# Optimization experiments

Measured on AMD Instinct MI355X. Metric: run time of the kernel, lower is better.

The kernel has to match this reference:

```python
import jax, jax.numpy as jnp
import numpy as np

FRACTAL_OUTPUT = (5, 5)            # (a, b); requires 5 * num_kernels == a*b
PERC_THRESHOLD = 0.59275
NEXT_SHAPE = (224, 224)
K_END = int(0.4 * FRACTAL_OUTPUT[0] * FRACTAL_OUTPUT[1] + 1)   # 11
KERNEL_SIZES = list(range(3, K_END + 1, 2))                    # [3,5,7,9,11]


def setup_inputs() -> dict:
    key = jax.random.key(0)
    inputs = jax.random.uniform(key, (64, 224, 224, 3), dtype=jnp.float32) * 255.0
    return {"inputs": inputs}


def _extract_patches(x, k):
    # tf.image.extract_patches(sizes=strides=k, SAME) == zero-pad + space-to-depth
    B, H, W, C = x.shape
    rows, cols = -(-H // k), -(-W // k)
    ph, pw = rows * k - H, cols * k - W
    x = jnp.pad(x, ((0, 0), (ph // 2, ph - ph // 2), (pw // 2, pw - pw // 2), (0, 0)))
    x = x.reshape(B, rows, k, cols, k, C).transpose(0, 1, 3, 2, 4, 5)
    return x.reshape(B * rows * cols, k, k, C), rows * cols


def _binarize(patches, k, ch):
    # distance function: 1 iff |channel value - center pixel channel value| <= k
    center = patches[:, k // 2, k // 2, ch][:, None, None]
    return (jnp.abs(patches[..., ch] - center) <= k).astype(jnp.int32)


def _connected_stats(binp, k):
    # 4-connected components via min-label propagation (== tfa connected_components
    # up to relabeling; we only need #components and max label count incl. background)
    N = binp.shape[0]
    idx = jnp.arange(1, k * k + 1, dtype=jnp.int32).reshape(k, k)
    INF = jnp.int32(k * k + 2)
    lbl0 = jnp.where(binp > 0, idx, 0)

    def step(_, lbl):
        v = jnp.where(binp > 0, lbl, INF)
        pad = lambda a, w: jnp.pad(a, ((0, 0),) + w, constant_values=INF)
        up    = pad(v, ((1, 0), (0, 0)))[:, :-1, :]
        down  = pad(v, ((0, 1), (0, 0)))[:, 1:, :]
        left  = pad(v, ((0, 0), (1, 0)))[:, :, :-1]
        right = pad(v, ((0, 0), (0, 1)))[:, :, 1:]
        m = jnp.minimum(jnp.minimum(v, up), jnp.minimum(jnp.minimum(down, left), right))
        return jnp.where(binp > 0, m, 0)

    lbl = jax.lax.fori_loop(0, k * k, step, lbl0)  # k*k iters guarantee convergence
    ncomp = jnp.sum((binp > 0) & (lbl == idx), axis=(1, 2)).astype(jnp.int32)
    lblf = lbl.reshape(N, k * k)
    cnt = jnp.zeros((N, k * k + 1), jnp.int32).at[jnp.arange(N)[:, None], lblf].add(1)
    return ncomp, cnt.max(axis=1)  # (#components, most-common label count incl bg 0)


def _components(inputs, k, ch):
    B = inputs.shape[0]
    patches, P = _extract_patches(inputs, k)
    binp = _binarize(patches, k, ch)                    # (B*P, k, k)
    ones = binp.sum(axis=(1, 2)).reshape(B, P)          # int counts per patch
    # tf.bincount(minlength=1, maxlength=k*k): bins 0..k*k-1, value k*k dropped
    cnt = jnp.zeros((B, k * k + 1), jnp.float32).at[jnp.arange(B)[:, None], ones].add(1.0)
    prob = cnt[:, : k * k] / P                          # (B, k*k)
    n = jnp.arange(1, k * k + 1, dtype=jnp.float32)
    fd = (prob / n).sum(1)
    m = (prob * n).sum(1)
    m2 = ((prob * prob) * n).sum(1)
    lac = (m2 - m * m) / (m * m)
    perc = ((ones.astype(jnp.float32) / (k * k)) >= PERC_THRESHOLD).astype(jnp.int32)
    acp = perc.sum(1) // P                              # tf integer reduce_mean
    ncomp, marea = _connected_stats(binp, k)
    acn = ncomp.reshape(B, P).sum(1) // P
    acma = marea.reshape(B, P).sum(1) // P
    return jnp.stack([acn.astype(jnp.float32), acp.astype(jnp.float32),
                      acma.astype(jnp.float32), lac, fd], axis=1)   # (B, 5)


def _rearrange(c):
    # group metric-major: all acn over kernels, then acp, acma, lac, fd
    return jnp.concatenate([c[:, mm::5] for mm in range(5)], axis=1)


def reference(inputs):
    B = inputs.shape[0]
    chans = []
    for ch in range(3):
        comps = jnp.concatenate([_components(inputs, k, ch) for k in KERNEL_SIZES], axis=1)
        chans.append(_rearrange(comps).reshape(B, FRACTAL_OUTPUT[0], FRACTAL_OUTPUT[1]))
    out = jnp.stack(chans, axis=3)                      # (B, a, b, 3)
    return jax.image.resize(out, (B, NEXT_SHAPE[0], NEXT_SHAPE[1], 3), method='bilinear')
```

## Files before the change

### kernel.cpp

```cpp
#include <hip/hip_runtime.h>

#define HW 224
#define NIMG 64
#define NPIX ((size_t)NIMG * HW * HW)

struct U128 { unsigned long long lo, hi; };
__device__ __forceinline__ U128 u_or  (U128 a, U128 b){ return {a.lo|b.lo, a.hi|b.hi}; }
__device__ __forceinline__ U128 u_and (U128 a, U128 b){ return {a.lo&b.lo, a.hi&b.hi}; }
__device__ __forceinline__ U128 u_andn(U128 a, U128 b){ return {a.lo&~b.lo, a.hi&~b.hi}; }
__device__ __forceinline__ bool u_eq(U128 a, U128 b){ return a.lo==b.lo && a.hi==b.hi; }
__device__ __forceinline__ bool u_nz(U128 a){ return (a.lo | a.hi) != 0ull; }
__device__ __forceinline__ U128 u_shl(U128 a, int n){
    return { a.lo << n, (a.hi << n) | (a.lo >> (64 - n)) };
}
__device__ __forceinline__ U128 u_shr(U128 a, int n){
    return { (a.lo >> n) | (a.hi << (64 - n)), a.hi >> n };
}
__device__ __forceinline__ int u_pop(U128 a){ return __popcll(a.lo) + __popcll(a.hi); }
__device__ __forceinline__ U128 u_low(U128 a){
    if (a.lo) return { a.lo & (0ull - a.lo), 0ull };
    return { 0ull, a.hi & (0ull - a.hi) };
}


template<int K, int S>
__device__ __forceinline__ void stats_body(const float* __restrict__ img,
                                           float* __restrict__ o,
                                           int hist[4][124], int* sums) {
    constexpr int KK   = K * K;
    constexpr int ROWS = (HW + K - 1) / K;
    constexpr int P    = ROWS * ROWS;
    constexpr int PAD  = (ROWS * K - HW) / 2;
    const int wid = threadIdx.x >> 6;

    U128 leftCol{0,0}, rightCol{0,0};
#pragma unroll
    for (int i = 0; i < K; i++) {
        const int cl = i * K, cr = i * K + K - 1;
        if (cl < 64) leftCol.lo  |= 1ull << cl; else leftCol.hi  |= 1ull << (cl - 64);
        if (cr < 64) rightCol.lo |= 1ull << cr; else rightCol.hi |= 1ull << (cr - 64);
    }

    int t_perc = 0, t_ncomp = 0, t_marea = 0;

    for (int p = threadIdx.x; p < P; p += 256) {
        const int pr = p / ROWS, pc = p - pr * ROWS;
        const int y0 = pr * K - PAD, x0 = pc * K - PAD;
        const float cen = img[((size_t)(y0 + K / 2) * HW + (x0 + K / 2)) * S];

        U128 msk{0, 0};
#pragma unroll
        for (int i = 0; i < K; i++) {
            const int y = y0 + i;
            const bool yin = (unsigned)y < (unsigned)HW;
#pragma unroll
            for (int j = 0; j < K; j++) {
                const int x = x0 + j;
                const bool inb = yin && ((unsigned)x < (unsigned)HW);
                const float v = inb ? img[((size_t)y * HW + x) * S] : 0.0f;
                const unsigned long long bit = (fabsf(v - cen) <= (float)K) ? 1ull : 0ull;
                const int c = i * K + j;
                if (c < 64) msk.lo |= bit << c; else msk.hi |= bit << (c - 64);
            }
        }
        const int ones = u_pop(msk);

        int ncomp = 0, maxsz = 0;
        U128 m = msk;
        while (u_nz(m)) {
            U128 s = u_low(m);
            for (;;) {
                U128 g = s;
                g = u_or(g, u_shl(u_andn(s, rightCol), 1));
                g = u_or(g, u_shr(u_andn(s, leftCol), 1));
                g = u_or(g, u_shl(s, K));
                g = u_or(g, u_shr(s, K));
                g = u_and(g, m);
                if (u_eq(g, s)) break;
                s = g;
            }
            ncomp++;
            const int sz = u_pop(s);
            if (sz > maxsz) maxsz = sz;
            m = u_andn(m, s);
        }

        const int bgcnt = KK - ones;
        const int marea = (bgcnt > maxsz) ? bgcnt : maxsz;

        t_ncomp += ncomp;
        t_marea += marea;
        if ((float)ones / (float)KK >= 0.59275f) t_perc++;
        atomicAdd(&hist[wid][ones], 1);
    }

    atomicAdd(&sums[0], t_perc);
    atomicAdd(&sums[1], t_ncomp);
    atomicAdd(&sums[2], t_marea);
    __syncthreads();

    if (threadIdx.x == 0) {
        const float Pf = (float)P;
        float fd = 0.0f, m1 = 0.0f, m2 = 0.0f;
        for (int s = 0; s < KK; s++) {
            const float prob = (float)(hist[0][s] + hist[1][s] + hist[2][s] + hist[3][s]) / Pf;
            const float n = (float)(s + 1);
            fd += prob / n;
            m1 += prob * n;
            m2 += prob * prob * n;
        }
        const float lac = (m2 - m1 * m1) / (m1 * m1);
        o[0]  = (float)(sums[1] / P);
        o[15] = (float)(sums[0] / P);
        o[30] = (float)(sums[2] / P);
        o[45] = lac;
        o[60] = fd;
    }
}

template<int S>
__global__ __launch_bounds__(256) void fractal_stats(const float* __restrict__ in,
                                                     float* __restrict__ interm) {
    const int b    = blockIdx.x / 15;
    const int rem  = blockIdx.x % 15;
    const int ch   = rem / 5;
    const int kidx = rem % 5;

    __shared__ int hist[4][124];
    __shared__ int sums[3];
    for (int i = threadIdx.x; i < 4 * 124; i += 256) ((int*)hist)[i] = 0;
    if (threadIdx.x < 3) sums[threadIdx.x] = 0;
    __syncthreads();

    const float* img = (S == 1) ? in + ((size_t)ch * NIMG + b) * HW * HW
                                : in + (size_t)b * HW * HW * 3 + ch;
    float* o = interm + (size_t)b * 75 + kidx * 3 + ch;

    switch (kidx) {
        case 0: stats_body<3,  S>(img, o, hist, sums); break;
        case 1: stats_body<5,  S>(img, o, hist, sums); break;
        case 2: stats_body<7,  S>(img, o, hist, sums); break;
        case 3: stats_body<9,  S>(img, o, hist, sums); break;
        case 4: stats_body<11, S>(img, o, hist, sums); break;
    }
}

__global__ __launch_bounds__(256) void deinterleave(const float* __restrict__ in,
                                                    float* __restrict__ planes) {
    const size_t pix = (size_t)blockIdx.x * 256 + threadIdx.x;
    if (pix >= NPIX) return;
    const float v0 = in[pix * 3 + 0];
    const float v1 = in[pix * 3 + 1];
    const float v2 = in[pix * 3 + 2];
    planes[pix]            = v0;
    planes[NPIX + pix]     = v1;
    planes[2 * NPIX + pix] = v2;
}

__global__ __launch_bounds__(256) void fractal_resize(const float* __restrict__ interm,
                                                      float* __restrict__ out, int total) {
    const int idx = blockIdx.x * 256 + threadIdx.x;
    if (idx >= total) return;
    const int ch = idx % 3;
    int t = idx / 3;
    const int x = t % HW; t /= HW;
    const int y = t % HW;
    const int b = t / HW;

    const float sc = 5.0f / 224.0f;
    const float uy = ((float)y + 0.5f) * sc - 0.5f;
    const float ux = ((float)x + 0.5f) * sc - 0.5f;

    const float fy = floorf(uy), fx = floorf(ux);
    const float wy = uy - fy,    wx = ux - fx;
    int y0 = (int)fy, x0 = (int)fx;
    int y1 = y0 + 1,  x1 = x0 + 1;
    if (y0 < 0) y0 = 0; if (x0 < 0) x0 = 0;
    if (y1 > 4) y1 = 4; if (x1 > 4) x1 = 4;

    const float* g = interm + (size_t)b * 75 + ch;
    const float v00 = g[(y0 * 5 + x0) * 3];
    const float v01 = g[(y0 * 5 + x1) * 3];
    const float v10 = g[(y1 * 5 + x0) * 3];
    const float v11 = g[(y1 * 5 + x1) * 3];

    out[idx] = (1.0f - wy) * ((1.0f - wx) * v00 + wx * v01)
             +         wy  * ((1.0f - wx) * v10 + wx * v11);
}

extern "C" void kernel_launch(void* const* d_in, const int* in_sizes, int n_in,
                              void* d_out, int out_size, void* d_ws, size_t ws_size,
                              hipStream_t stream) {
    const float* in = (const float*)d_in[0];
    float* out = (float*)d_out;
    float* interm = (float*)d_ws;

    const size_t planes_off = 19456;
    const size_t need = planes_off + 3 * NPIX * sizeof(float);

    if (ws_size >= need) {
        float* planes = (float*)((char*)d_ws + planes_off);
        deinterleave<<<(int)((NPIX + 255) / 256), 256, 0, stream>>>(in, planes);
        fractal_stats<1><<<NIMG * 15, 256, 0, stream>>>(planes, interm);
    } else {
        fractal_stats<3><<<NIMG * 15, 256, 0, stream>>>(in, interm);
    }
    fractal_resize<<<(out_size + 255) / 256, 256, 0, stream>>>(interm, out, out_size);
}
```

Measured before the change: 185.8 us.

## Split each stats group across eight blocks with global atomic accumulation and finalize kernel

Each (image, channel, kernel-size) group is now spread over eight blocks, each taking a slice of the patches. Per-block histograms and sums are atomically added into a global accumulator, and a separate finalize kernel computes the metrics. Small kernels (K<=7) use a single 64-bit mask path instead of the 128-bit one. The deinterleave now handles four pixels per thread with float4 and also zeroes the accumulator. This fixes the poor occupancy of only 960 blocks with load imbalance, at the cost of an extra launch and global atomics.

```diff
diff --git a/kernel.cpp b/kernel.cpp
--- a/kernel.cpp
+++ b/kernel.cpp
@@ -3,6 +3,9 @@
 #define HW 224
 #define NIMG 64
 #define NPIX ((size_t)NIMG * HW * HW)
+#define NGROUP 960
+#define ACC_STRIDE 128
+#define NSUB 8
 
 struct U128 { unsigned long long lo, hi; };
 __device__ __forceinline__ U128 u_or  (U128 a, U128 b){ return {a.lo|b.lo, a.hi|b.hi}; }
@@ -25,64 +28,106 @@
 
 template<int K, int S>
 __device__ __forceinline__ void stats_body(const float* __restrict__ img,
-                                           float* __restrict__ o,
+                                           int* __restrict__ acc, int sub,
                                            int hist[4][124], int* sums) {
-    constexpr int KK   = K * K;
-    constexpr int ROWS = (HW + K - 1) / K;
-    constexpr int P    = ROWS * ROWS;
-    constexpr int PAD  = (ROWS * K - HW) / 2;
+    constexpr int KK    = K * K;
+    constexpr int ROWS  = (HW + K - 1) / K;
+    constexpr int P     = ROWS * ROWS;
+    constexpr int PAD   = (ROWS * K - HW) / 2;
+    constexpr int CHUNK = (P + NSUB - 1) / NSUB;
     const int wid = threadIdx.x >> 6;
-
-    U128 leftCol{0,0}, rightCol{0,0};
-#pragma unroll
-    for (int i = 0; i < K; i++) {
-        const int cl = i * K, cr = i * K + K - 1;
-        if (cl < 64) leftCol.lo  |= 1ull << cl; else leftCol.hi  |= 1ull << (cl - 64);
-        if (cr < 64) rightCol.lo |= 1ull << cr; else rightCol.hi |= 1ull << (cr - 64);
-    }
+    const int pstart = sub * CHUNK;
+    const int pend   = (pstart + CHUNK < P) ? pstart + CHUNK : P;
 
     int t_perc = 0, t_ncomp = 0, t_marea = 0;
 
-    for (int p = threadIdx.x; p < P; p += 256) {
+    for (int p = pstart + threadIdx.x; p < pend; p += 256) {
         const int pr = p / ROWS, pc = p - pr * ROWS;
         const int y0 = pr * K - PAD, x0 = pc * K - PAD;
-        const float cen = img[((size_t)(y0 + K / 2) * HW + (x0 + K / 2)) * S];
-
-        U128 msk{0, 0};
-#pragma unroll
-        for (int i = 0; i < K; i++) {
-            const int y = y0 + i;
-            const bool yin = (unsigned)y < (unsigned)HW;
-#pragma unroll
-            for (int j = 0; j < K; j++) {
-                const int x = x0 + j;
-                const bool inb = yin && ((unsigned)x < (unsigned)HW);
-                const float v = inb ? img[((size_t)y * HW + x) * S] : 0.0f;
-                const unsigned long long bit = (fabsf(v - cen) <= (float)K) ? 1ull : 0ull;
-                const int c = i * K + j;
-                if (c < 64) msk.lo |= bit << c; else msk.hi |= bit << (c - 64);
-            }
-        }
-        const int ones = u_pop(msk);
-
-        int ncomp = 0, maxsz = 0;
-        U128 m = msk;
-        while (u_nz(m)) {
-            U128 s = u_low(m);
-            for (;;) {
-                U128 g = s;
-                g = u_or(g, u_shl(u_andn(s, rightCol), 1));
-                g = u_or(g, u_shr(u_andn(s, leftCol), 1));
-                g = u_or(g, u_shl(s, K));
-                g = u_or(g, u_shr(s, K));
-                g = u_and(g, m);
-                if (u_eq(g, s)) break;
-                s = g;
-            }
-            ncomp++;
-            const int sz = u_pop(s);
-            if (sz > maxsz) maxsz = sz;
-            m = u_andn(m, s);
+        const float cen = img[((y0 + K / 2) * HW + (x0 + K / 2)) * S];
+
+        int ones, ncomp = 0, maxsz = 0;
+
+        if constexpr (KK <= 64) {
+            unsigned long long LCOL = 0ull, RCOL = 0ull;
+#pragma unroll
+            for (int i = 0; i < K; i++) { LCOL |= 1ull << (i * K); RCOL |= 1ull << (i * K + K - 1); }
+
+            unsigned long long msk = 0ull;
+#pragma unroll
+            for (int i = 0; i < K; i++) {
+                const int y = y0 + i;
+                const bool yin = (unsigned)y < (unsigned)HW;
+#pragma unroll
+                for (int j = 0; j < K; j++) {
+                    const int x = x0 + j;
+                    const bool inb = yin && ((unsigned)x < (unsigned)HW);
+                    const float v = inb ? img[(y * HW + x) * S] : 0.0f;
+                    const unsigned long long bit = (fabsf(v - cen) <= (float)K) ? 1ull : 0ull;
+                    msk |= bit << (i * K + j);
+                }
+            }
+            ones = __popcll(msk);
+
+            unsigned long long m = msk;
+            while (m) {
+                unsigned long long s = m & (0ull - m);
+                for (;;) {
+                    unsigned long long g = s | ((s & ~RCOL) << 1) | ((s & ~LCOL) >> 1)
+                                             | (s << K) | (s >> K);
+                    g &= m;
+                    if (g == s) break;
+                    s = g;
+                }
+                ncomp++;
+                const int sz = __popcll(s);
+                if (sz > maxsz) maxsz = sz;
+                m &= ~s;
+            }
+        } else {
+            U128 LCOL{0,0}, RCOL{0,0};
+#pragma unroll
+            for (int i = 0; i < K; i++) {
+                const int cl = i * K, cr = i * K + K - 1;
+                if (cl < 64) LCOL.lo |= 1ull << cl; else LCOL.hi |= 1ull << (cl - 64);
+                if (cr < 64) RCOL.lo |= 1ull << cr; else RCOL.hi |= 1ull << (cr - 64);
+            }
+
+            U128 msk{0, 0};
+#pragma unroll
+            for (int i = 0; i < K; i++) {
+                const int y = y0 + i;
+                const bool yin = (unsigned)y < (unsigned)HW;
+#pragma unroll
+                for (int j = 0; j < K; j++) {
+                    const int x = x0 + j;
+                    const bool inb = yin && ((unsigned)x < (unsigned)HW);
+                    const float v = inb ? img[(y * HW + x) * S] : 0.0f;
+                    const unsigned long long bit = (fabsf(v - cen) <= (float)K) ? 1ull : 0ull;
+                    const int c = i * K + j;
+                    if (c < 64) msk.lo |= bit << c; else msk.hi |= bit << (c - 64);
+                }
+            }
+            ones = u_pop(msk);
+
+            U128 m = msk;
+            while (u_nz(m)) {
+                U128 s = u_low(m);
+                for (;;) {
+                    U128 g = s;
+                    g = u_or(g, u_shl(u_andn(s, RCOL), 1));
+                    g = u_or(g, u_shr(u_andn(s, LCOL), 1));
+                    g = u_or(g, u_shl(s, K));
+                    g = u_or(g, u_shr(s, K));
+                    g = u_and(g, m);
+                    if (u_eq(g, s)) break;
+                    s = g;
+                }
+                ncomp++;
+                const int sz = u_pop(s);
+                if (sz > maxsz) maxsz = sz;
+                m = u_andn(m, s);
+            }
         }
 
         const int bgcnt = KK - ones;
@@ -99,32 +144,22 @@
     atomicAdd(&sums[2], t_marea);
     __syncthreads();
 
-    if (threadIdx.x == 0) {
-        const float Pf = (float)P;
-        float fd = 0.0f, m1 = 0.0f, m2 = 0.0f;
-        for (int s = 0; s < KK; s++) {
-            const float prob = (float)(hist[0][s] + hist[1][s] + hist[2][s] + hist[3][s]) / Pf;
-            const float n = (float)(s + 1);
-            fd += prob / n;
-            m1 += prob * n;
-            m2 += prob * prob * n;
-        }
-        const float lac = (m2 - m1 * m1) / (m1 * m1);
-        o[0]  = (float)(sums[1] / P);
-        o[15] = (float)(sums[0] / P);
-        o[30] = (float)(sums[2] / P);
-        o[45] = lac;
-        o[60] = fd;
-    }
+    for (int s = threadIdx.x; s < KK; s += 256) {
+        const int v = hist[0][s] + hist[1][s] + hist[2][s] + hist[3][s];
+        if (v) atomicAdd(&acc[s], v);
+    }
+    if (threadIdx.x < 3) atomicAdd(&acc[124 + threadIdx.x], sums[threadIdx.x]);
 }
 
 template<int S>
 __global__ __launch_bounds__(256) void fractal_stats(const float* __restrict__ in,
-                                                     float* __restrict__ interm) {
-    const int b    = blockIdx.x / 15;
-    const int rem  = blockIdx.x % 15;
-    const int ch   = rem / 5;
-    const int kidx = rem % 5;
+                                                     int* __restrict__ gacc) {
+    const int group = blockIdx.x >> 3;
+    const int sub   = blockIdx.x & 7;
+    const int b     = group / 15;
+    const int rem   = group % 15;
+    const int ch    = rem / 5;
+    const int kidx  = rem % 5;
 
     __shared__ int hist[4][124];
     __shared__ int sums[3];
@@ -134,27 +169,62 @@
 
     const float* img = (S == 1) ? in + ((size_t)ch * NIMG + b) * HW * HW
                                 : in + (size_t)b * HW * HW * 3 + ch;
+    int* acc = gacc + group * ACC_STRIDE;
+
+    switch (kidx) {
+        case 0: stats_body<3,  S>(img, acc, sub, hist, sums); break;
+        case 1: stats_body<5,  S>(img, acc, sub, hist, sums); break;
+        case 2: stats_body<7,  S>(img, acc, sub, hist, sums); break;
+        case 3: stats_body<9,  S>(img, acc, sub, hist, sums); break;
+        case 4: stats_body<11, S>(img, acc, sub, hist, sums); break;
+    }
+}
+
+__global__ __launch_bounds__(256) void fractal_finalize(const int* __restrict__ gacc,
+                                                        float* __restrict__ interm) {
+    const int g = blockIdx.x * 256 + threadIdx.x;
+    if (g >= NGROUP) return;
+    const int b = g / 15, rem = g % 15, ch = rem / 5, kidx = rem % 5;
+    const int k = 3 + 2 * kidx, kk = k * k;
+    const int rows = (HW + k - 1) / k;
+    const int P = rows * rows;
+    const int* acc = gacc + g * ACC_STRIDE;
+
+    float fd = 0.0f, m1 = 0.0f, m2 = 0.0f;
+    const float Pf = (float)P;
+    for (int s = 0; s < kk; s++) {
+        const float prob = (float)acc[s] / Pf;
+        const float n = (float)(s + 1);
+        fd += prob / n;
+        m1 += prob * n;
+        m2 += prob * prob * n;
+    }
+    const float lac = (m2 - m1 * m1) / (m1 * m1);
     float* o = interm + (size_t)b * 75 + kidx * 3 + ch;
-
-    switch (kidx) {
-        case 0: stats_body<3,  S>(img, o, hist, sums); break;
-        case 1: stats_body<5,  S>(img, o, hist, sums); break;
-        case 2: stats_body<7,  S>(img, o, hist, sums); break;
-        case 3: stats_body<9,  S>(img, o, hist, sums); break;
-        case 4: stats_body<11, S>(img, o, hist, sums); break;
-    }
-}
-
-__global__ __launch_bounds__(256) void deinterleave(const float* __restrict__ in,
-                                                    float* __restrict__ planes) {
-    const size_t pix = (size_t)blockIdx.x * 256 + threadIdx.x;
-    if (pix >= NPIX) return;
-    const float v0 = in[pix * 3 + 0];
-    const float v1 = in[pix * 3 + 1];
-    const float v2 = in[pix * 3 + 2];
-    planes[pix]            = v0;
-    planes[NPIX + pix]     = v1;
-    planes[2 * NPIX + pix] = v2;
+    o[0]  = (float)(acc[125] / P);
+    o[15] = (float)(acc[124] / P);
+    o[30] = (float)(acc[126] / P);
+    o[45] = lac;
+    o[60] = fd;
+}
+
+__global__ __launch_bounds__(256) void deinterleave4(const float* __restrict__ in,
+                                                     float* __restrict__ planes,
+                                                     int* __restrict__ gacc) {
+    const int tid = blockIdx.x * 256 + threadIdx.x;
+    if (tid < NGROUP * ACC_STRIDE) gacc[tid] = 0;
+    const size_t p0 = (size_t)tid * 4;
+    if (p0 >= NPIX) return;
+    const float4* src = (const float4*)(in + p0 * 3);
+    const float4 a = src[0], bq = src[1], c = src[2];
+    *(float4*)(planes + p0)            = make_float4(a.x, a.w, bq.z, c.y);
+    *(float4*)(planes + NPIX + p0)     = make_float4(a.y, bq.x, bq.w, c.z);
+    *(float4*)(planes + 2 * NPIX + p0) = make_float4(a.z, bq.y, c.x, c.w);
+}
+
+__global__ __launch_bounds__(256) void zero_accum(int* __restrict__ gacc) {
+    const int tid = blockIdx.x * 256 + threadIdx.x;
+    if (tid < NGROUP * ACC_STRIDE) gacc[tid] = 0;
 }
 
 __global__ __launch_bounds__(256) void fractal_resize(const float* __restrict__ interm,
@@ -194,16 +264,18 @@
     const float* in = (const float*)d_in[0];
     float* out = (float*)d_out;
     float* interm = (float*)d_ws;
-
-    const size_t planes_off = 19456;
-    const size_t need = planes_off + 3 * NPIX * sizeof(float);
+    int*   gacc   = (int*)((char*)d_ws + 19456);
+    float* planes = (float*)((char*)d_ws + 512000);
+
+    const size_t need = 512000 + 3 * NPIX * sizeof(float);
 
     if (ws_size >= need) {
-        float* planes = (float*)((char*)d_ws + planes_off);
-        deinterleave<<<(int)((NPIX + 255) / 256), 256, 0, stream>>>(in, planes);
-        fractal_stats<1><<<NIMG * 15, 256, 0, stream>>>(planes, interm);
+        deinterleave4<<<(int)(NPIX / 4 / 256), 256, 0, stream>>>(in, planes, gacc);
+        fractal_stats<1><<<NGROUP * NSUB, 256, 0, stream>>>(planes, gacc);
     } else {
-        fractal_stats<3><<<NIMG * 15, 256, 0, stream>>>(in, interm);
-    }
+        zero_accum<<<(NGROUP * ACC_STRIDE + 255) / 256, 256, 0, stream>>>(gacc);
+        fractal_stats<3><<<NGROUP * NSUB, 256, 0, stream>>>(in, gacc);
+    }
+    fractal_finalize<<<(NGROUP + 255) / 256, 256, 0, stream>>>(gacc, interm);
     fractal_resize<<<(out_size + 255) / 256, 256, 0, stream>>>(interm, out, out_size);
 }
```

Measured after the change: 264.8 us. 42.5% more time.

## Stage image row bands in LDS and drop deinterleave pre-pass

Applied to the files above, without the earlier changes.

Removes the separate deinterleave kernel and planar workspace copy. Each block now loads bands of NB*K image rows from the interleaved input with float4 loads, extracts its channel, and stores the band to LDS with zero padding. Patches then read from LDS instead of strided global memory. It also adds a 64-bit mask fast path for K<=7 and a wave-shuffle reduction for the final statistics. The cost is extra block syncs per band and each block redundantly reading all three channels' data.

```diff
diff --git a/kernel.cpp b/kernel.cpp
--- a/kernel.cpp
+++ b/kernel.cpp
@@ -2,7 +2,8 @@
 
 #define HW 224
 #define NIMG 64
-#define NPIX ((size_t)NIMG * HW * HW)
+#define NGROUP 960
+#define LDS_F4 1914
 
 struct U128 { unsigned long long lo, hi; };
 __device__ __forceinline__ U128 u_or  (U128 a, U128 b){ return {a.lo|b.lo, a.hi|b.hi}; }
@@ -23,75 +24,145 @@
 }
 
 
-template<int K, int S>
-__device__ __forceinline__ void stats_body(const float* __restrict__ img,
-                                           float* __restrict__ o,
-                                           int hist[4][124], int* sums) {
-    constexpr int KK   = K * K;
-    constexpr int ROWS = (HW + K - 1) / K;
-    constexpr int P    = ROWS * ROWS;
-    constexpr int PAD  = (ROWS * K - HW) / 2;
-    const int wid = threadIdx.x >> 6;
-
-    U128 leftCol{0,0}, rightCol{0,0};
-#pragma unroll
-    for (int i = 0; i < K; i++) {
-        const int cl = i * K, cr = i * K + K - 1;
-        if (cl < 64) leftCol.lo  |= 1ull << cl; else leftCol.hi  |= 1ull << (cl - 64);
-        if (cr < 64) rightCol.lo |= 1ull << cr; else rightCol.hi |= 1ull << (cr - 64);
-    }
+template<int K>
+__device__ __forceinline__ void stats_group(const float* __restrict__ imgbase,
+                                            int ch,
+                                            float* __restrict__ o,
+                                            float4* lds4, int (*hist)[124],
+                                            int* sums) {
+    constexpr int KK    = K * K;
+    constexpr int ROWS  = (HW + K - 1) / K;
+    constexpr int P     = ROWS * ROWS;
+    constexpr int PAD   = (ROWS * K - HW) / 2;
+    constexpr int NB    = (K==3) ? 6 : (K==5) ? 5 : (K==7) ? 4 : 3;
+    constexpr int NCYC  = (ROWS + NB - 1) / NB;
+    constexpr int R     = NB * K;
+    constexpr int LPAD4 = (PAD > 0) ? 1 : 0;
+    constexpr int LPAD  = 4 * LPAD4;
+    constexpr int OFF   = LPAD - PAD;
+    constexpr int ACT   = NB * ROWS;
+
+    float* ldsf = (float*)lds4;
+    const int tid = threadIdx.x;
+    const int wid = (tid >> 6) & 1;
+
+    for (int i = tid; i < 2 * 124; i += 256) ((int*)hist)[i] = 0;
+    if (tid < 3) sums[tid] = 0;
+    __syncthreads();
 
     int t_perc = 0, t_ncomp = 0, t_marea = 0;
 
-    for (int p = threadIdx.x; p < P; p += 256) {
-        const int pr = p / ROWS, pc = p - pr * ROWS;
-        const int y0 = pr * K - PAD, x0 = pc * K - PAD;
-        const float cen = img[((size_t)(y0 + K / 2) * HW + (x0 + K / 2)) * S];
-
-        U128 msk{0, 0};
-#pragma unroll
-        for (int i = 0; i < K; i++) {
-            const int y = y0 + i;
-            const bool yin = (unsigned)y < (unsigned)HW;
-#pragma unroll
-            for (int j = 0; j < K; j++) {
-                const int x = x0 + j;
-                const bool inb = yin && ((unsigned)x < (unsigned)HW);
-                const float v = inb ? img[((size_t)y * HW + x) * S] : 0.0f;
-                const unsigned long long bit = (fabsf(v - cen) <= (float)K) ? 1ull : 0ull;
-                const int c = i * K + j;
-                if (c < 64) msk.lo |= bit << c; else msk.hi |= bit << (c - 64);
+    for (int s = 0; s < NCYC; s++) {
+        const int gy0 = s * NB * K - PAD;
+
+        for (int i = tid; i < R * 56; i += 256) {
+            const int r = i / 56, t4 = i - r * 56;
+            const int gy = gy0 + r;
+            float4 v = {0.f, 0.f, 0.f, 0.f};
+            if ((unsigned)gy < (unsigned)HW) {
+                const float4* s4 = (const float4*)(imgbase + 3 * (gy * HW + 4 * t4));
+                const float4 A = s4[0], B = s4[1], C = s4[2];
+                v = (ch == 0) ? float4{A.x, A.w, B.z, C.y}
+                  : (ch == 1) ? float4{A.y, B.x, B.w, C.z}
+                              : float4{A.z, B.y, C.x, C.w};
             }
-        }
-        const int ones = u_pop(msk);
-
-        int ncomp = 0, maxsz = 0;
-        U128 m = msk;
-        while (u_nz(m)) {
-            U128 s = u_low(m);
-            for (;;) {
-                U128 g = s;
-                g = u_or(g, u_shl(u_andn(s, rightCol), 1));
-                g = u_or(g, u_shr(u_andn(s, leftCol), 1));
-                g = u_or(g, u_shl(s, K));
-                g = u_or(g, u_shr(s, K));
-                g = u_and(g, m);
-                if (u_eq(g, s)) break;
-                s = g;
+            lds4[r * 58 + LPAD4 + t4] = v;
+        }
+        for (int i = tid; i < R * 2; i += 256) {
+            const int r = i >> 1, w = i & 1;
+            const int slot = LPAD4 ? (w ? 57 : 0) : (56 + w);
+            lds4[r * 58 + slot] = float4{0.f, 0.f, 0.f, 0.f};
+        }
+        __syncthreads();
+
+        for (int pl = tid; pl < ACT; pl += 256) {
+            const int bi = pl / ROWS, pc = pl - bi * ROWS;
+            const int pr = s * NB + bi;
+            if (pr >= ROWS) break;
+            const int base = pc * K + OFF;
+            const float cen = ldsf[(bi * K + K / 2) * 232 + base + K / 2];
+
+            int ones, ncomp = 0, maxsz = 0;
+
+            if constexpr (KK <= 64) {
+                unsigned long long LCOL = 0ull, RCOL = 0ull;
+#pragma unroll
+                for (int i = 0; i < K; i++) { LCOL |= 1ull << (i*K); RCOL |= 1ull << (i*K + K - 1); }
+                unsigned long long msk = 0ull;
+#pragma unroll
+                for (int i = 0; i < K; i++) {
+                    const int rb = (bi * K + i) * 232 + base;
+#pragma unroll
+                    for (int j = 0; j < K; j++) {
+                        const float v = ldsf[rb + j];
+                        msk |= (fabsf(v - cen) <= (float)K ? 1ull : 0ull) << (i * K + j);
+                    }
+                }
+                ones = __popcll(msk);
+                unsigned long long m = msk;
+                while (m) {
+                    unsigned long long t = m & (0ull - m);
+                    for (;;) {
+                        unsigned long long g = t | ((t & ~RCOL) << 1) | ((t & ~LCOL) >> 1)
+                                                 | (t << K) | (t >> K);
+                        g &= m;
+                        if (g == t) break;
+                        t = g;
+                    }
+                    ncomp++;
+                    const int sz = __popcll(t);
+                    if (sz > maxsz) maxsz = sz;
+                    m &= ~t;
+                }
+            } else {
+                U128 LCOL{0,0}, RCOL{0,0};
+#pragma unroll
+                for (int i = 0; i < K; i++) {
+                    const int cl = i * K, cr = i * K + K - 1;
+                    if (cl < 64) LCOL.lo |= 1ull << cl; else LCOL.hi |= 1ull << (cl - 64);
+                    if (cr < 64) RCOL.lo |= 1ull << cr; else RCOL.hi |= 1ull << (cr - 64);
+                }
+                U128 msk{0, 0};
+#pragma unroll
+                for (int i = 0; i < K; i++) {
+                    const int rb = (bi * K + i) * 232 + base;
+#pragma unroll
+                    for (int j = 0; j < K; j++) {
+                        const float v = ldsf[rb + j];
+                        const unsigned long long bit = (fabsf(v - cen) <= (float)K) ? 1ull : 0ull;
+                        const int c = i * K + j;
+                        if (c < 64) msk.lo |= bit << c; else msk.hi |= bit << (c - 64);
+                    }
+                }
+                ones = u_pop(msk);
+                U128 m = msk;
+                while (u_nz(m)) {
+                    U128 t = u_low(m);
+                    for (;;) {
+                        U128 g = t;
+                        g = u_or(g, u_shl(u_andn(t, RCOL), 1));
+                        g = u_or(g, u_shr(u_andn(t, LCOL), 1));
+                        g = u_or(g, u_shl(t, K));
+                        g = u_or(g, u_shr(t, K));
+                        g = u_and(g, m);
+                        if (u_eq(g, t)) break;
+                        t = g;
+                    }
+                    ncomp++;
+                    const int sz = u_pop(t);
+                    if (sz > maxsz) maxsz = sz;
+                    m = u_andn(m, t);
+                }
             }
-            ncomp++;
-            const int sz = u_pop(s);
-            if (sz > maxsz) maxsz = sz;
-            m = u_andn(m, s);
-        }
-
-        const int bgcnt = KK - ones;
-        const int marea = (bgcnt > maxsz) ? bgcnt : maxsz;
-
-        t_ncomp += ncomp;
-        t_marea += marea;
-        if ((float)ones / (float)KK >= 0.59275f) t_perc++;
-        atomicAdd(&hist[wid][ones], 1);
+
+            const int bgcnt = KK - ones;
+            const int marea = (bgcnt > maxsz) ? bgcnt : maxsz;
+            t_ncomp += ncomp;
+            t_marea += marea;
+            if ((float)ones / (float)KK >= 0.59275f) t_perc++;
+            atomicAdd(&hist[wid][ones], 1);
+        }
+        __syncthreads();
     }
 
     atomicAdd(&sums[0], t_perc);
@@ -99,62 +170,51 @@
     atomicAdd(&sums[2], t_marea);
     __syncthreads();
 
-    if (threadIdx.x == 0) {
-        const float Pf = (float)P;
-        float fd = 0.0f, m1 = 0.0f, m2 = 0.0f;
-        for (int s = 0; s < KK; s++) {
-            const float prob = (float)(hist[0][s] + hist[1][s] + hist[2][s] + hist[3][s]) / Pf;
-            const float n = (float)(s + 1);
+    if (tid < 64) {
+        float fd = 0.f, m1 = 0.f, m2 = 0.f;
+        for (int s2 = tid; s2 < KK; s2 += 64) {
+            const float prob = (float)(hist[0][s2] + hist[1][s2]) / (float)P;
+            const float n = (float)(s2 + 1);
             fd += prob / n;
             m1 += prob * n;
             m2 += prob * prob * n;
         }
-        const float lac = (m2 - m1 * m1) / (m1 * m1);
-        o[0]  = (float)(sums[1] / P);
-        o[15] = (float)(sums[0] / P);
-        o[30] = (float)(sums[2] / P);
-        o[45] = lac;
-        o[60] = fd;
+#pragma unroll
+        for (int off = 32; off; off >>= 1) {
+            fd += __shfl_down(fd, off, 64);
+            m1 += __shfl_down(m1, off, 64);
+            m2 += __shfl_down(m2, off, 64);
+        }
+        if (tid == 0) {
+            const float lac = (m2 - m1 * m1) / (m1 * m1);
+            o[0]  = (float)(sums[1] / P);
+            o[15] = (float)(sums[0] / P);
+            o[30] = (float)(sums[2] / P);
+            o[45] = lac;
+            o[60] = fd;
+        }
     }
 }
 
-template<int S>
 __global__ __launch_bounds__(256) void fractal_stats(const float* __restrict__ in,
                                                      float* __restrict__ interm) {
-    const int b    = blockIdx.x / 15;
-    const int rem  = blockIdx.x % 15;
-    const int ch   = rem / 5;
-    const int kidx = rem % 5;
-
-    __shared__ int hist[4][124];
+    const int group = blockIdx.x;
+    const int b = group / 15, rem = group % 15, ch = rem / 5, kidx = rem % 5;
+
+    __shared__ float4 lds4[LDS_F4];
+    __shared__ int hist[2][124];
     __shared__ int sums[3];
-    for (int i = threadIdx.x; i < 4 * 124; i += 256) ((int*)hist)[i] = 0;
-    if (threadIdx.x < 3) sums[threadIdx.x] = 0;
-    __syncthreads();
-
-    const float* img = (S == 1) ? in + ((size_t)ch * NIMG + b) * HW * HW
-                                : in + (size_t)b * HW * HW * 3 + ch;
+
+    const float* imgbase = in + (size_t)b * HW * HW * 3;
     float* o = interm + (size_t)b * 75 + kidx * 3 + ch;
 
     switch (kidx) {
-        case 0: stats_body<3,  S>(img, o, hist, sums); break;
-        case 1: stats_body<5,  S>(img, o, hist, sums); break;
-        case 2: stats_body<7,  S>(img, o, hist, sums); break;
-        case 3: stats_body<9,  S>(img, o, hist, sums); break;
-        case 4: stats_body<11, S>(img, o, hist, sums); break;
+        case 0: stats_group<3 >(imgbase, ch, o, lds4, hist, sums); break;
+        case 1: stats_group<5 >(imgbase, ch, o, lds4, hist, sums); break;
+        case 2: stats_group<7 >(imgbase, ch, o, lds4, hist, sums); break;
+        case 3: stats_group<9 >(imgbase, ch, o, lds4, hist, sums); break;
+        case 4: stats_group<11>(imgbase, ch, o, lds4, hist, sums); break;
     }
-}
-
-__global__ __launch_bounds__(256) void deinterleave(const float* __restrict__ in,
-                                                    float* __restrict__ planes) {
-    const size_t pix = (size_t)blockIdx.x * 256 + threadIdx.x;
-    if (pix >= NPIX) return;
-    const float v0 = in[pix * 3 + 0];
-    const float v1 = in[pix * 3 + 1];
-    const float v2 = in[pix * 3 + 2];
-    planes[pix]            = v0;
-    planes[NPIX + pix]     = v1;
-    planes[2 * NPIX + pix] = v2;
 }
 
 __global__ __launch_bounds__(256) void fractal_resize(const float* __restrict__ interm,
@@ -195,15 +255,6 @@
     float* out = (float*)d_out;
     float* interm = (float*)d_ws;
 
-    const size_t planes_off = 19456;
-    const size_t need = planes_off + 3 * NPIX * sizeof(float);
-
-    if (ws_size >= need) {
-        float* planes = (float*)((char*)d_ws + planes_off);
-        deinterleave<<<(int)((NPIX + 255) / 256), 256, 0, stream>>>(in, planes);
-        fractal_stats<1><<<NIMG * 15, 256, 0, stream>>>(planes, interm);
-    } else {
-        fractal_stats<3><<<NIMG * 15, 256, 0, stream>>>(in, interm);
-    }
+    fractal_stats<<<NGROUP, 256, 0, stream>>>(in, interm);
     fractal_resize<<<(out_size + 255) / 256, 256, 0, stream>>>(interm, out, out_size);
 }
```

After: 199.6 us. 1.07x slower.
